# Kernel optimization log

Hardware: AMD Instinct MI355X
Metric: run time of the kernel (lower is better)

Reference implementation:

```python
import jax, jax.numpy as jnp
import numpy as np

N = 4096; B = 4; NPB = N // B; K = 16
C = 128; COUT = 128; LMAX = 2; L = (LMAX + 1) ** 2  # 9 SH coefficients
H = 8; A = 8; V = 16; HV = H * V
F = 256; NB = 128; FD = 256; CUTOFF = 3.0
E = N * K

def _silu(x):
    return x * jax.nn.sigmoid(x)

def _mish(x):
    return x * jnp.tanh(jax.nn.softplus(x))

def _rms_norm(x, gamma):
    # degree-wise RMS over channel dim, x: [N, L, C]
    s = jnp.sqrt(jnp.mean(x * x, axis=-1, keepdims=True) + 1e-6)
    return x / s * gamma

def _rot_l1(x, R):
    # rotate the l=1 block (coeffs 1:4) of x [E, L, C] by R [E, 3, 3]
    l1 = jnp.einsum('eij,ejc->eic', R, x[:, 1:4, :])
    return jnp.concatenate([x[:, :1, :], l1, x[:, 4:, :]], axis=1)

def _knn(coord, batch):
    d2 = jnp.sum((coord[:, None, :] - coord[None, :, :]) ** 2, axis=-1)  # [N,N]
    same = batch[:, None] == batch[None, :]
    big = jnp.asarray(1e9, d2.dtype)
    d2 = jnp.where(same, d2, big)
    d2 = d2.at[jnp.arange(N), jnp.arange(N)].set(big)
    neg, idx = jax.lax.top_k(-d2, K)
    dist = jnp.sqrt(jnp.maximum(-neg, 0.0))
    edge_src = idx.reshape(-1)                       # [E]
    edge_dst = jnp.repeat(jnp.arange(N), K)          # [E]
    valid = (dist <= CUTOFF).reshape(-1)
    return edge_src, edge_dst, valid

def _edge_rot_mat(edge_vec):
    # deterministic rotation aligning each edge with the y-axis (eSCN-style)
    nx = edge_vec / (jnp.linalg.norm(edge_vec, axis=-1, keepdims=True) + 1e-12)
    ref = jnp.where(jnp.abs(nx[:, :1]) < 0.9,
                    jnp.array([1.0, 0.0, 0.0], nx.dtype),
                    jnp.array([0.0, 1.0, 0.0], nx.dtype))
    nz = jnp.cross(nx, ref)
    nz = nz / (jnp.linalg.norm(nz, axis=-1, keepdims=True) + 1e-12)
    ny = jnp.cross(nz, nx)
    return jnp.stack([nz, nx, ny], axis=1)  # [E,3,3]; R @ edge_dir = e_y

def _forward(node_coord, node_emb, batch, condition,
             W_e1, b_e1, W_e2, b_e2, W_src, W_dst, w_a, W_v, W_o,
             gamma1, gamma2, W_g, W_f1, W_f2, W_film, b_film):
    # dynamic KNN graph; geometry detached as in original (edge_vec.detach())
    coord_g = jax.lax.stop_gradient(node_coord)
    edge_src, edge_dst, valid = _knn(coord_g, batch)
    edge_vec = coord_g[edge_src] - coord_g[edge_dst]                  # [E,3]
    edge_len = jnp.linalg.norm(edge_vec, axis=-1)                     # [E]
    R = _edge_rot_mat(edge_vec)                                       # [E,3,3]
    # gaussian radial basis -> per-edge embedding
    mu = jnp.linspace(0.0, CUTOFF, NB)
    sigma = CUTOFF / NB
    rbf = jnp.exp(-0.5 * ((edge_len[:, None] - mu) / sigma) ** 2)     # [E,NB]
    edge_h = _silu(rbf @ W_e1 + b_e1) @ W_e2 + b_e2                   # [E,HV]
    # equivariant attention (rotate into edge frame, attend, rotate back)
    x_src = _rot_l1(node_emb[edge_src], R)                            # [E,L,C]
    q = node_emb[edge_dst, 0] @ W_dst + x_src[:, 0] @ W_src           # [E,H*A]
    logits = jnp.einsum('eha,ha->eh', _silu(q).reshape(E, H, A), w_a)
    logits = jnp.where(valid[:, None], logits, -1e9)
    m = jax.ops.segment_max(logits, edge_dst, num_segments=N)
    ex = jnp.exp(logits - m[edge_dst])
    den = jax.ops.segment_sum(ex, edge_dst, num_segments=N)
    attn = ex / (den[edge_dst] + 1e-9)                                # [E,H]
    v = jnp.einsum('elc,cv->elv', x_src, W_v) * edge_h[:, None, :]    # [E,L,HV]
    v = v.reshape(E, L, H, V) * attn[:, None, :, None]
    msg = _rot_l1(v.reshape(E, L, HV), jnp.swapaxes(R, 1, 2))         # back to global frame
    agg = jax.ops.segment_sum(msg, edge_dst, num_segments=N)          # [N,L,HV]
    x = node_emb + jnp.einsum('nlv,vc->nlc', agg, W_o)
    # FFN with separable S2 (scalar-gated) activation
    h = _rms_norm(x, gamma2)
    gate = _silu(h[:, 0] @ W_g)                                       # [N,F]
    hid = jnp.einsum('nlc,cf->nlf', h, W_f1) * gate[:, None, :]
    x = x + jnp.einsum('nlf,fo->nlo', hid, W_f2)
    x = _rms_norm(x, gamma1)
    # FiLM conditioning over flattened (L*C) per batch element
    film = _mish(condition) @ W_film + b_film                         # [B, 2*L*COUT]
    w, bfi = film[:, :L * COUT], film[:, L * COUT:]
    c = x.reshape(B, NPB, L * COUT) * w[:, None, :] + bfi[:, None, :]
    return c.reshape(N, L, COUT)

def setup_inputs():
    key = jax.random.key(0)
    ks = jax.random.split(key, 16)
    node_coord = jax.random.uniform(ks[0], (N, 3)) * 2.0
    node_emb = jax.random.normal(ks[1], (N, L, C)) * 0.1
    batch = jnp.arange(N, dtype=jnp.int64 if jax.config.jax_enable_x64 else jnp.int32) // NPB
    condition = jax.random.normal(ks[2], (B, FD))
    s = lambda d: 1.0 / np.sqrt(d)
    return {
        'node_coord': node_coord, 'node_emb': node_emb, 'batch': batch, 'condition': condition,
        'W_e1': jax.random.normal(ks[3], (NB, 128)) * s(NB), 'b_e1': jnp.zeros((128,)),
        'W_e2': jax.random.normal(ks[4], (128, HV)) * s(128), 'b_e2': jnp.zeros((HV,)),
        'W_src': jax.random.normal(ks[5], (C, H * A)) * s(C),
        'W_dst': jax.random.normal(ks[6], (C, H * A)) * s(C),
        'w_a': jax.random.normal(ks[7], (H, A)) * s(A),
        'W_v': jax.random.normal(ks[8], (C, HV)) * s(C),
        'W_o': jax.random.normal(ks[9], (HV, C)) * s(HV),
        'gamma1': jnp.ones((C,)), 'gamma2': jnp.ones((C,)),
        'W_g': jax.random.normal(ks[10], (C, F)) * s(C),
        'W_f1': jax.random.normal(ks[11], (C, F)) * s(C),
        'W_f2': jax.random.normal(ks[12], (F, COUT)) * s(F),
        'W_film': jax.random.normal(ks[13], (FD, 2 * L * COUT)) * s(FD),
        'b_film': jnp.zeros((2 * L * COUT,)),
    }

def reference(node_coord, node_emb, batch, condition,
              W_e1, b_e1, W_e2, b_e2, W_src, W_dst, w_a, W_v, W_o,
              gamma1, gamma2, W_g, W_f1, W_f2, W_film, b_film):
    out = _forward(node_coord, node_emb, batch, condition,
                   W_e1, b_e1, W_e2, b_e2, W_src, W_dst, w_a, W_v, W_o,
                   gamma1, gamma2, W_g, W_f1, W_f2, W_film, b_film)
    return (node_coord, out, batch)
```

## Files before the change

### kernel.cpp

```cpp
#include <hip/hip_runtime.h>

#define NNODE 4096
#define NPB   1024

typedef float v2f __attribute__((ext_vector_type(2)));
typedef float v4f __attribute__((ext_vector_type(4)));

__device__ __forceinline__ float siluf(float x){ return x / (1.0f + expf(-x)); }

__device__ __forceinline__ v2f pk_fma_lo(v2f a, v2f b, v2f c){
  v2f d;
  asm("v_pk_fma_f32 %0, %1, %2, %3 op_sel_hi:[1,0,1]" : "=v"(d) : "v"(a), "v"(b), "v"(c));
  return d;
}
__device__ __forceinline__ v2f pk_fma_hi(v2f a, v2f b, v2f c){
  v2f d;
  asm("v_pk_fma_f32 %0, %1, %2, %3 op_sel:[0,1,0] op_sel_hi:[1,1,1]" : "=v"(d) : "v"(a), "v"(b), "v"(c));
  return d;
}
__device__ __forceinline__ v2f pk_fma2(v2f a, v2f b, v2f c){
  v2f d;
  asm("v_pk_fma_f32 %0, %1, %2, %3" : "=v"(d) : "v"(a), "v"(b), "v"(c));
  return d;
}
#define SHLO(h) __builtin_shufflevector((h), (h), 0, 1)
#define SHHI(h) __builtin_shufflevector((h), (h), 2, 3)

__global__ __launch_bounds__(256) void k_film(const float* __restrict__ cond,
                                              const float* __restrict__ Wfilm,
                                              const float* __restrict__ bfilm,
                                              float* __restrict__ filmG){
  __shared__ float mL[256];
  int b = blockIdx.y;
  int t = threadIdx.x;
  int j = blockIdx.x*256 + t;
  float x = cond[b*256 + t];
  float sp = fmaxf(x, 0.f) + log1pf(expf(-fabsf(x)));
  mL[t] = x * tanhf(sp);
  __syncthreads();
  if(j >= 2304) return;
  float acc = bfilm[j];
  for(int i=0;i<256;i++) acc += mL[i] * Wfilm[i*2304 + j];
  filmG[b*2304 + j] = acc;
}

__global__ __launch_bounds__(256) void k_pre(const float* __restrict__ emb,
                                             const float* __restrict__ Wv,
                                             const float* __restrict__ Wsrc,
                                             const float* __restrict__ Wdst,
                                             float* __restrict__ ZG,
                                             float* __restrict__ QsG,
                                             float* __restrict__ QdG){
  __shared__ __align__(16) float S[4*1152];
  const int t = threadIdx.x;
  const int rg = __builtin_amdgcn_readfirstlane(t >> 6);
  const int lane = t & 63;
  const int c0 = lane*2;
  const int n0 = blockIdx.x*4;
  const int n = n0 + rg;

  {
    const float4* src = (const float4*)(emb + (size_t)n0*1152);
    float4* dst = (float4*)S;
    for(int i=t; i<1152; i+=256) dst[i] = src[i];
  }
  __syncthreads();
  const float* en = &S[rg*1152];

  v2f z[9];
  #pragma unroll
  for(int l=0;l<9;l++) z[l] = (v2f)0.0f;
  for(int c4=0;c4<32;c4++){
    v2f wv0 = *(const v2f*)&Wv[(c4*4+0)*128 + c0];
    v2f wv1 = *(const v2f*)&Wv[(c4*4+1)*128 + c0];
    v2f wv2 = *(const v2f*)&Wv[(c4*4+2)*128 + c0];
    v2f wv3 = *(const v2f*)&Wv[(c4*4+3)*128 + c0];
    #pragma unroll
    for(int l=0;l<9;l++){
      v4f x4 = *(const v4f*)&en[l*128 + c4*4];
      v2f h01 = SHLO(x4), h23 = SHHI(x4);
      z[l] = pk_fma_lo(wv0, h01, z[l]);
      z[l] = pk_fma_hi(wv1, h01, z[l]);
      z[l] = pk_fma_lo(wv2, h23, z[l]);
      z[l] = pk_fma_hi(wv3, h23, z[l]);
    }
  }
  #pragma unroll
  for(int l=0;l<9;l++) *(v2f*)&ZG[(size_t)n*1152 + l*128 + c0] = z[l];

  float qs = 0.f, qd = 0.f;
  for(int c4=0;c4<32;c4++){
    v4f e4 = *(const v4f*)&en[c4*4];
    qs = fmaf(e4.x, Wsrc[(c4*4+0)*64 + lane], qs);
    qs = fmaf(e4.y, Wsrc[(c4*4+1)*64 + lane], qs);
    qs = fmaf(e4.z, Wsrc[(c4*4+2)*64 + lane], qs);
    qs = fmaf(e4.w, Wsrc[(c4*4+3)*64 + lane], qs);
    qd = fmaf(e4.x, Wdst[(c4*4+0)*64 + lane], qd);
    qd = fmaf(e4.y, Wdst[(c4*4+1)*64 + lane], qd);
    qd = fmaf(e4.z, Wdst[(c4*4+2)*64 + lane], qd);
    qd = fmaf(e4.w, Wdst[(c4*4+3)*64 + lane], qd);
  }
  QsG[n*64 + lane] = qs;
  QdG[n*64 + lane] = qd;
}

#define E2_HD   0
#define E2_RB   2048
#define E2_AT   2304
#define E2_KI   2432
#define E2_LEN  2448
#define E2_VL   2464
#define E2_W0   2480
#define F_ACT   0
#define F_HID   1152
#define E2_NPF  2560
__global__ __launch_bounds__(128, 4) void k_node(
    const float* __restrict__ coord,
    const float* __restrict__ emb,
    const float* __restrict__ We1, const float* __restrict__ be1,
    const float* __restrict__ We2, const float* __restrict__ be2,
    const float* __restrict__ wa,
    const float* __restrict__ Wo,
    const float* __restrict__ g1, const float* __restrict__ g2,
    const float* __restrict__ Wg, const float* __restrict__ Wf1,
    const float* __restrict__ Wf2,
    const float* __restrict__ Qs, const float* __restrict__ Qd,
    const float* __restrict__ Z,
    const float* __restrict__ filmG,
    float* __restrict__ out){
  __shared__ __align__(16) float S[2*E2_NPF];
  int* Si = (int*)S;
  const int t = threadIdx.x;
  const int w = __builtin_amdgcn_readfirstlane(t >> 6);
  const int lane = t & 63;
  const int bid = blockIdx.x;
  const int sbid = (bid & 7) * (NNODE/16) + (bid >> 3);
  const int n = sbid*2 + w;
  const int base = n & ~(NPB - 1);
  const int self = n - base;
  const int NP = w * E2_NPF;
  const int c0 = lane*2;
  const int myh = lane >> 3;

  {
    const float* cb = coord + (size_t)base*3;
    const float cx = cb[self*3+0];
    const float cy = cb[self*3+1];
    const float cz = cb[self*3+2];
    float d2a[16]; int ida[16];
    #pragma unroll
    for(int q=0;q<16;q++){
      int j = lane + q*64;
      float dx = __fsub_rn(cb[j*3+0], cx);
      float dy = __fsub_rn(cb[j*3+1], cy);
      float dz = __fsub_rn(cb[j*3+2], cz);
      float d2 = __fadd_rn(__fadd_rn(__fmul_rn(dx,dx), __fmul_rn(dy,dy)), __fmul_rn(dz,dz));
      if(j == self) d2 = 3e38f;
      d2a[q] = d2; ida[q] = j;
    }
    #pragma unroll 1
    for(int r=0;r<16;r++){
      float bd = d2a[0]; int bi = ida[0];
      #pragma unroll
      for(int q=1;q<16;q++){
        bool bet = (d2a[q] < bd) || (d2a[q] == bd && ida[q] < bi);
        if(bet){ bd = d2a[q]; bi = ida[q]; }
      }
      #pragma unroll
      for(int s=1;s<64;s<<=1){
        float od = __shfl_xor(bd, s, 64);
        int   oi = __shfl_xor(bi, s, 64);
        bool bet = (od < bd) || (od == bd && oi < bi);
        if(bet){ bd = od; bi = oi; }
      }
      if(lane == 0){
        Si[NP + E2_KI + r] = bi;
        float len = __fsqrt_rn(bd);
        S[NP + E2_LEN + r] = len;
        S[NP + E2_VL + r]  = (len <= 3.0f) ? 1.0f : 0.0f;
        int i0 = (int)(len * (127.0f/3.0f) + 0.5f);
        int w0 = i0 - 7;
        w0 = w0 < 0 ? 0 : (w0 > 112 ? 112 : w0);
        Si[NP + E2_W0 + r] = w0;
      }
      #pragma unroll
      for(int q=0;q<16;q++) if(ida[q] == bi) d2a[q] = 3e38f;
    }
  }
  __syncthreads();

  {
    const int e0 = lane >> 3, hh = lane & 7;
    float4 qda = *(const float4*)&Qd[(size_t)n*64 + hh*8];
    float4 qdb = *(const float4*)&Qd[(size_t)n*64 + hh*8 + 4];
    float4 waa = *(const float4*)&wa[hh*8];
    float4 wab = *(const float4*)&wa[hh*8 + 4];
    float lg[2];
    #pragma unroll
    for(int s=0;s<2;s++){
      int e = e0 + s*8;
      int src = base + Si[NP + E2_KI + e];
      float4 qa = *(const float4*)&Qs[(size_t)src*64 + hh*8];
      float4 qb = *(const float4*)&Qs[(size_t)src*64 + hh*8 + 4];
      float sv = siluf(qda.x+qa.x)*waa.x + siluf(qda.y+qa.y)*waa.y
               + siluf(qda.z+qa.z)*waa.z + siluf(qda.w+qa.w)*waa.w
               + siluf(qdb.x+qb.x)*wab.x + siluf(qdb.y+qb.y)*wab.y
               + siluf(qdb.z+qb.z)*wab.z + siluf(qdb.w+qb.w)*wab.w;
      lg[s] = (S[NP + E2_VL + e] > 0.5f) ? sv : -1e9f;
    }
    float m = fmaxf(lg[0], lg[1]);
    m = fmaxf(m, __shfl_xor(m, 8, 64));
    m = fmaxf(m, __shfl_xor(m, 16, 64));
    m = fmaxf(m, __shfl_xor(m, 32, 64));
    float ex0 = expf(lg[0] - m), ex1 = expf(lg[1] - m);
    float den = ex0 + ex1;
    den += __shfl_xor(den, 8, 64);
    den += __shfl_xor(den, 16, 64);
    den += __shfl_xor(den, 32, 64);
    float inv = 1.0f/(den + 1e-9f);
    S[NP + E2_AT + lane]      = ex0*inv;
    S[NP + E2_AT + 64 + lane] = ex1*inv;

    const float step = 3.0f/127.0f;
    const float sigma = 3.0f/128.0f;
    #pragma unroll
    for(int k=0;k<4;k++){
      int idx = lane + k*64;
      int e = idx >> 4, wi = idx & 15;
      float len = S[NP + E2_LEN + e];
      int bin = Si[NP + E2_W0 + e] + wi;
      float d = (len - step*(float)bin) / sigma;
      S[NP + E2_RB + idx] = expf(-0.5f*d*d);
    }
  }
  __syncthreads();

  {
    float a4[16][2]; int b0e[16];
    #pragma unroll
    for(int e=0;e<16;e++){ a4[e][0]=0.f; a4[e][1]=0.f; b0e[e] = Si[NP + E2_W0 + e]; }
    #pragma unroll 1
    for(int wi=0; wi<16; wi++){
      #pragma unroll
      for(int e=0;e<16;e++){
        float rb = S[NP + E2_RB + e*16 + wi];
        float2 we = *(const float2*)&We1[(size_t)(b0e[e] + wi)*128 + c0];
        a4[e][0] = fmaf(rb, we.x, a4[e][0]);
        a4[e][1] = fmaf(rb, we.y, a4[e][1]);
      }
    }
    float2 b1v = *(const float2*)&be1[c0];
    #pragma unroll
    for(int e=0;e<16;e++){
      float2 o; o.x = siluf(a4[e][0] + b1v.x); o.y = siluf(a4[e][1] + b1v.y);
      *(float2*)&S[NP + E2_HD + e*128 + c0] = o;
    }
  }
  __syncthreads();

  v2f a5[16];
  #pragma unroll
  for(int e=0;e<16;e++) a5[e] = (v2f)0.0f;
  #pragma unroll 1
  for(int c4=0;c4<32;c4++){
    v2f w0 = *(const v2f*)&We2[(c4*4+0)*128 + c0];
    v2f w1 = *(const v2f*)&We2[(c4*4+1)*128 + c0];
    v2f w2 = *(const v2f*)&We2[(c4*4+2)*128 + c0];
    v2f w3 = *(const v2f*)&We2[(c4*4+3)*128 + c0];
    #pragma unroll
    for(int e=0;e<16;e++){
      v4f h4 = *(const v4f*)&S[NP + E2_HD + e*128 + c4*4];
      v2f h01 = SHLO(h4), h23 = SHHI(h4);
      a5[e] = pk_fma_lo(w0, h01, a5[e]);
      a5[e] = pk_fma_hi(w1, h01, a5[e]);
      a5[e] = pk_fma_lo(w2, h23, a5[e]);
      a5[e] = pk_fma_hi(w3, h23, a5[e]);
    }
  }

  {
    v2f b2v = *(const v2f*)&be2[c0];
    v2f ag[9];
    #pragma unroll
    for(int l=0;l<9;l++) ag[l] = (v2f)0.0f;
    #pragma unroll 4
    for(int e=0;e<16;e++){
      int src = base + Si[NP + E2_KI + e];
      const float* zp = &Z[(size_t)src*1152 + c0];
      float at = S[NP + E2_AT + e*8 + myh];
      v2f sc = (a5[e] + b2v) * at;
      #pragma unroll
      for(int l=0;l<9;l++){
        v2f z2 = *(const v2f*)&zp[l*128];
        ag[l] = pk_fma2(z2, sc, ag[l]);
      }
    }
    #pragma unroll
    for(int l=0;l<9;l++) *(v2f*)&S[NP + F_ACT + l*128 + c0] = ag[l];
  }

  float* W_ = &S[NP];

  v2f x[9];
  #pragma unroll
  for(int l=0;l<9;l++) x[l] = (v2f)0.0f;
  #pragma unroll 1
  for(int c4=0;c4<32;c4++){
    v2f w0 = *(const v2f*)&Wo[(c4*4+0)*128 + c0];
    v2f w1 = *(const v2f*)&Wo[(c4*4+1)*128 + c0];
    v2f w2 = *(const v2f*)&Wo[(c4*4+2)*128 + c0];
    v2f w3 = *(const v2f*)&Wo[(c4*4+3)*128 + c0];
    #pragma unroll
    for(int l=0;l<9;l++){
      v4f a4 = *(const v4f*)&W_[F_ACT + l*128 + c4*4];
      v2f h01 = SHLO(a4), h23 = SHHI(a4);
      x[l] = pk_fma_lo(w0, h01, x[l]);
      x[l] = pk_fma_hi(w1, h01, x[l]);
      x[l] = pk_fma_lo(w2, h23, x[l]);
      x[l] = pk_fma_hi(w3, h23, x[l]);
    }
  }

  {
    float g2a = g2[c0], g2b = g2[c0+1];
    #pragma unroll
    for(int l=0;l<9;l++){
      v2f e2 = *(const v2f*)&emb[(size_t)n*1152 + l*128 + c0];
      x[l] += e2;
      float sq = x[l][0]*x[l][0] + x[l][1]*x[l][1];
      #pragma unroll
      for(int s=1;s<64;s<<=1) sq += __shfl_xor(sq, s, 64);
      float ss = sqrtf(sq/128.f + 1e-6f);
      v2f o; o.x = x[l][0]/ss*g2a; o.y = x[l][1]/ss*g2b;
      *(v2f*)&W_[F_ACT + l*128 + c0] = o;
    }
  }

  #pragma unroll 1
  for(int ft=0;ft<2;ft++){
    v2f ha[9]; v2f ga = (v2f)0.0f;
    #pragma unroll
    for(int l=0;l<9;l++) ha[l] = (v2f)0.0f;
    #pragma unroll 1
    for(int c4=0;c4<32;c4++){
      v2f wf0 = *(const v2f*)&Wf1[(c4*4+0)*256 + ft*128 + c0];
      v2f wf1 = *(const v2f*)&Wf1[(c4*4+1)*256 + ft*128 + c0];
      v2f wf2 = *(const v2f*)&Wf1[(c4*4+2)*256 + ft*128 + c0];
      v2f wf3 = *(const v2f*)&Wf1[(c4*4+3)*256 + ft*128 + c0];
      v2f wg0 = *(const v2f*)&Wg [(c4*4+0)*256 + ft*128 + c0];
      v2f wg1 = *(const v2f*)&Wg [(c4*4+1)*256 + ft*128 + c0];
      v2f wg2 = *(const v2f*)&Wg [(c4*4+2)*256 + ft*128 + c0];
      v2f wg3 = *(const v2f*)&Wg [(c4*4+3)*256 + ft*128 + c0];
      v4f h0 = *(const v4f*)&W_[F_ACT + 0*128 + c4*4];
      v2f h01 = SHLO(h0), h23 = SHHI(h0);
      ga = pk_fma_lo(wg0, h01, ga);
      ga = pk_fma_hi(wg1, h01, ga);
      ga = pk_fma_lo(wg2, h23, ga);
      ga = pk_fma_hi(wg3, h23, ga);
      ha[0] = pk_fma_lo(wf0, h01, ha[0]);
      ha[0] = pk_fma_hi(wf1, h01, ha[0]);
      ha[0] = pk_fma_lo(wf2, h23, ha[0]);
      ha[0] = pk_fma_hi(wf3, h23, ha[0]);
      #pragma unroll
      for(int l=1;l<9;l++){
        v4f h4 = *(const v4f*)&W_[F_ACT + l*128 + c4*4];
        v2f a01 = SHLO(h4), a23 = SHHI(h4);
        ha[l] = pk_fma_lo(wf0, a01, ha[l]);
        ha[l] = pk_fma_hi(wf1, a01, ha[l]);
        ha[l] = pk_fma_lo(wf2, a23, ha[l]);
        ha[l] = pk_fma_hi(wf3, a23, ha[l]);
      }
    }
    float gx = siluf(ga[0]), gy = siluf(ga[1]);
    #pragma unroll
    for(int l=0;l<9;l++){
      v2f o; o.x = ha[l][0]*gx; o.y = ha[l][1]*gy;
      *(v2f*)&W_[F_HID + l*128 + c0] = o;
    }
    #pragma unroll 1
    for(int f4=0;f4<32;f4++){
      v2f w0 = *(const v2f*)&Wf2[(ft*128 + f4*4+0)*128 + c0];
      v2f w1 = *(const v2f*)&Wf2[(ft*128 + f4*4+1)*128 + c0];
      v2f w2 = *(const v2f*)&Wf2[(ft*128 + f4*4+2)*128 + c0];
      v2f w3 = *(const v2f*)&Wf2[(ft*128 + f4*4+3)*128 + c0];
      #pragma unroll
      for(int l=0;l<9;l++){
        v4f h4 = *(const v4f*)&W_[F_HID + l*128 + f4*4];
        v2f h01 = SHLO(h4), h23 = SHHI(h4);
        x[l] = pk_fma_lo(w0, h01, x[l]);
        x[l] = pk_fma_hi(w1, h01, x[l]);
        x[l] = pk_fma_lo(w2, h23, x[l]);
        x[l] = pk_fma_hi(w3, h23, x[l]);
      }
    }
  }

  {
    float g1a = g1[c0], g1b = g1[c0+1];
    int b = n >> 10;
    #pragma unroll
    for(int l=0;l<9;l++){
      float sq = x[l][0]*x[l][0] + x[l][1]*x[l][1];
      #pragma unroll
      for(int s=1;s<64;s<<=1) sq += __shfl_xor(sq, s, 64);
      float ss = sqrtf(sq/128.f + 1e-6f);
      v2f fw = *(const v2f*)&filmG[b*2304 + l*128 + c0];
      v2f fb = *(const v2f*)&filmG[b*2304 + 1152 + l*128 + c0];
      v2f o;
      o.x = x[l][0]/ss*g1a*fw.x + fb.x;
      o.y = x[l][1]/ss*g1b*fw.y + fb.y;
      *(v2f*)&out[12288 + (size_t)n*1152 + l*128 + c0] = o;
    }
  }
}

__global__ __launch_bounds__(256) void k_copy(const float* __restrict__ coord,
                                              float* __restrict__ out){
  int i = blockIdx.x*256 + threadIdx.x;
  if(i < 12288) out[i] = coord[i];
  int n = i - 12288;
  if(n >= 0 && n < 4096) out[12288 + 4718592 + n] = (float)(n >> 10);
}

extern "C" void kernel_launch(void* const* d_in, const int* in_sizes, int n_in,
                              void* d_out, int out_size, void* d_ws, size_t ws_size,
                              hipStream_t stream) {
  const float* coord = (const float*)d_in[0];
  const float* emb   = (const float*)d_in[1];
  const float* cond  = (const float*)d_in[3];
  const float* We1   = (const float*)d_in[4];
  const float* be1   = (const float*)d_in[5];
  const float* We2   = (const float*)d_in[6];
  const float* be2   = (const float*)d_in[7];
  const float* Wsrc  = (const float*)d_in[8];
  const float* Wdst  = (const float*)d_in[9];
  const float* wa    = (const float*)d_in[10];
  const float* Wv    = (const float*)d_in[11];
  const float* Wo    = (const float*)d_in[12];
  const float* g1    = (const float*)d_in[13];
  const float* g2    = (const float*)d_in[14];
  const float* Wg    = (const float*)d_in[15];
  const float* Wf1   = (const float*)d_in[16];
  const float* Wf2   = (const float*)d_in[17];
  const float* Wfilm = (const float*)d_in[18];
  const float* bfilm = (const float*)d_in[19];

  float* outf  = (float*)d_out;
  float* filmG = (float*)d_ws;
  float* QsG   = filmG + 9216;
  float* QdG   = QsG + 262144;
  float* ZG    = QdG + 262144;

  k_film<<<dim3(9,4), 256, 0, stream>>>(cond, Wfilm, bfilm, filmG);
  k_pre<<<NNODE/4, 256, 0, stream>>>(emb, Wv, Wsrc, Wdst, ZG, QsG, QdG);
  k_node<<<NNODE/2, 128, 0, stream>>>(coord, emb,
                                      We1, be1, We2, be2, wa,
                                      Wo, g1, g2, Wg, Wf1, Wf2,
                                      QsG, QdG, ZG, filmG, outf);
  k_copy<<<64, 256, 0, stream>>>(coord, outf);
}
```

Before: 361.3 us.

## Merge FiLM and copy kernels into neighbours and unroll node GEMM loops by two

The FiLM projection becomes extra blocks appended to the k_pre grid, and the coordinate/batch copy is folded into the tail of k_node, cutting the launch count from four to two. Separately, the inner GEMM loops in k_node change from unroll 1 to unroll 2 to expose more load/FMA overlap. The merged FiLM blocks share the grid with the heavier pre blocks, and the extra unrolling may raise register pressure and lower occupancy.

```diff
diff --git a/kernel.cpp b/kernel.cpp
--- a/kernel.cpp
+++ b/kernel.cpp
@@ -26,37 +26,41 @@
 #define SHLO(h) __builtin_shufflevector((h), (h), 0, 1)
 #define SHHI(h) __builtin_shufflevector((h), (h), 2, 3)
 
-__global__ __launch_bounds__(256) void k_film(const float* __restrict__ cond,
-                                              const float* __restrict__ Wfilm,
-                                              const float* __restrict__ bfilm,
-                                              float* __restrict__ filmG){
-  __shared__ float mL[256];
-  int b = blockIdx.y;
-  int t = threadIdx.x;
-  int j = blockIdx.x*256 + t;
-  float x = cond[b*256 + t];
-  float sp = fmaxf(x, 0.f) + log1pf(expf(-fabsf(x)));
-  mL[t] = x * tanhf(sp);
-  __syncthreads();
-  if(j >= 2304) return;
-  float acc = bfilm[j];
-  for(int i=0;i<256;i++) acc += mL[i] * Wfilm[i*2304 + j];
-  filmG[b*2304 + j] = acc;
-}
-
 __global__ __launch_bounds__(256) void k_pre(const float* __restrict__ emb,
                                              const float* __restrict__ Wv,
                                              const float* __restrict__ Wsrc,
                                              const float* __restrict__ Wdst,
+                                             const float* __restrict__ cond,
+                                             const float* __restrict__ Wfilm,
+                                             const float* __restrict__ bfilm,
                                              float* __restrict__ ZG,
                                              float* __restrict__ QsG,
-                                             float* __restrict__ QdG){
+                                             float* __restrict__ QdG,
+                                             float* __restrict__ filmG){
   __shared__ __align__(16) float S[4*1152];
   const int t = threadIdx.x;
+  const int bidx = blockIdx.x;
+
+  if(bidx >= 1024){
+    int fb = bidx - 1024;
+    int b  = fb / 9;
+    int jb = fb % 9;
+    int j  = jb*256 + t;
+    float x = cond[b*256 + t];
+    float sp = fmaxf(x, 0.f) + log1pf(expf(-fabsf(x)));
+    S[t] = x * tanhf(sp);
+    __syncthreads();
+    if(j >= 2304) return;
+    float acc = bfilm[j];
+    for(int i=0;i<256;i++) acc += S[i] * Wfilm[i*2304 + j];
+    filmG[b*2304 + j] = acc;
+    return;
+  }
+
   const int rg = __builtin_amdgcn_readfirstlane(t >> 6);
   const int lane = t & 63;
   const int c0 = lane*2;
-  const int n0 = blockIdx.x*4;
+  const int n0 = bidx*4;
   const int n = n0 + rg;
 
   {
@@ -239,7 +243,7 @@
     float a4[16][2]; int b0e[16];
     #pragma unroll
     for(int e=0;e<16;e++){ a4[e][0]=0.f; a4[e][1]=0.f; b0e[e] = Si[NP + E2_W0 + e]; }
-    #pragma unroll 1
+    #pragma unroll 2
     for(int wi=0; wi<16; wi++){
       #pragma unroll
       for(int e=0;e<16;e++){
@@ -261,7 +265,7 @@
   v2f a5[16];
   #pragma unroll
   for(int e=0;e<16;e++) a5[e] = (v2f)0.0f;
-  #pragma unroll 1
+  #pragma unroll 2
   for(int c4=0;c4<32;c4++){
     v2f w0 = *(const v2f*)&We2[(c4*4+0)*128 + c0];
     v2f w1 = *(const v2f*)&We2[(c4*4+1)*128 + c0];
@@ -304,7 +308,7 @@
   v2f x[9];
   #pragma unroll
   for(int l=0;l<9;l++) x[l] = (v2f)0.0f;
-  #pragma unroll 1
+  #pragma unroll 2
   for(int c4=0;c4<32;c4++){
     v2f w0 = *(const v2f*)&Wo[(c4*4+0)*128 + c0];
     v2f w1 = *(const v2f*)&Wo[(c4*4+1)*128 + c0];
@@ -341,7 +345,7 @@
     v2f ha[9]; v2f ga = (v2f)0.0f;
     #pragma unroll
     for(int l=0;l<9;l++) ha[l] = (v2f)0.0f;
-    #pragma unroll 1
+    #pragma unroll 2
     for(int c4=0;c4<32;c4++){
       v2f wf0 = *(const v2f*)&Wf1[(c4*4+0)*256 + ft*128 + c0];
       v2f wf1 = *(const v2f*)&Wf1[(c4*4+1)*256 + ft*128 + c0];
@@ -377,7 +381,7 @@
       v2f o; o.x = ha[l][0]*gx; o.y = ha[l][1]*gy;
       *(v2f*)&W_[F_HID + l*128 + c0] = o;
     }
-    #pragma unroll 1
+    #pragma unroll 2
     for(int f4=0;f4<32;f4++){
       v2f w0 = *(const v2f*)&Wf2[(ft*128 + f4*4+0)*128 + c0];
       v2f w1 = *(const v2f*)&Wf2[(ft*128 + f4*4+1)*128 + c0];
@@ -412,14 +416,9 @@
       *(v2f*)&out[12288 + (size_t)n*1152 + l*128 + c0] = o;
     }
   }
-}
-
-__global__ __launch_bounds__(256) void k_copy(const float* __restrict__ coord,
-                                              float* __restrict__ out){
-  int i = blockIdx.x*256 + threadIdx.x;
-  if(i < 12288) out[i] = coord[i];
-  int n = i - 12288;
-  if(n >= 0 && n < 4096) out[12288 + 4718592 + n] = (float)(n >> 10);
+
+  if(lane < 3) out[(size_t)n*3 + lane] = coord[(size_t)n*3 + lane];
+  if(lane == 3) out[12288 + 4718592 + n] = (float)(n >> 10);
 }
 
 extern "C" void kernel_launch(void* const* d_in, const int* in_sizes, int n_in,
@@ -451,11 +450,11 @@
   float* QdG   = QsG + 262144;
   float* ZG    = QdG + 262144;
 
-  k_film<<<dim3(9,4), 256, 0, stream>>>(cond, Wfilm, bfilm, filmG);
-  k_pre<<<NNODE/4, 256, 0, stream>>>(emb, Wv, Wsrc, Wdst, ZG, QsG, QdG);
+  k_pre<<<1024 + 36, 256, 0, stream>>>(emb, Wv, Wsrc, Wdst,
+                                       cond, Wfilm, bfilm,
+                                       ZG, QsG, QdG, filmG);
   k_node<<<NNODE/2, 128, 0, stream>>>(coord, emb,
                                       We1, be1, We2, be2, wa,
                                       Wo, g1, g2, Wg, Wf1, Wf2,
                                       QsG, QdG, ZG, filmG, outf);
-  k_copy<<<64, 256, 0, stream>>>(coord, outf);
-}
+}
```

Result: slower. 418.3 us (+15.8%).
